# Kernel tuning notes

Hardware: AMD Instinct MI355X
Metric: run time of the kernel (lower is better)

## Reference

```python
import jax, jax.numpy as jnp
import numpy as np

L, B = 1024, 64
VALID_FRAC = 0.9  # fraction of residues with nonzero (observed) coordinates in y


def setup_inputs() -> dict:
    key = jax.random.key(0)
    kx, ky = jax.random.split(key)
    x = jax.random.normal(kx, (L, B, 3), dtype=jnp.float32)
    y = jax.random.normal(ky, (L, B, 3), dtype=jnp.float32)
    # zero out trailing residues in y so the dynamic mask (co.sum() != 0) is exercised
    valid = (jnp.arange(L) < int(VALID_FRAC * L))[:, None, None]
    y = y * valid.astype(jnp.float32)
    return {"x": x, "y": y}


def _masked_pair_dist(pts, pair_mask):
    # pts: [B, L, 3]; pair_mask: [B, L, L] (False on diagonal and on padded rows/cols)
    sq = jnp.sum(pts * pts, axis=-1)                                   # [B, L]
    d2 = sq[:, :, None] + sq[:, None, :] - 2.0 * jnp.einsum('bld,bmd->blm', pts, pts)
    d2 = jnp.maximum(d2, 0.0)                                          # relu, matches F.relu
    safe = jnp.where(pair_mask, d2, 1.0)                               # keep sqrt grad finite
    return jnp.where(pair_mask, jnp.sqrt(safe), 0.0)


def reference(x, y):
    # x, y: [L, B, 3] -> permute to [B, L, 3] as in the torch module
    xb = jnp.transpose(x, (1, 0, 2))
    yb = jnp.transpose(y, (1, 0, 2))
    Bn, Ln = xb.shape[0], xb.shape[1]
    # mask: residues of y whose coordinate sum is nonzero (index_select in original)
    mask = (jnp.sum(yb, axis=-1) != 0)                                 # [B, L]
    off_diag = ~jnp.eye(Ln, dtype=bool)
    pair_mask = mask[:, :, None] & mask[:, None, :] & off_diag         # [B, L, L]
    xd = _masked_pair_dist(xb, pair_mask)
    yd = _masked_pair_dist(yb, pair_mask)
    D = yd - xd                                                        # [B, L, L]
    per_batch = jnp.sqrt(jnp.sum(D * D, axis=(1, 2)))                  # Frobenius norm per batch
    denom = (Ln ** 2 / 2 - Ln) ** 0.5                                  # x.size(1)**2/2 - x.size(1)
    out = jnp.sum(per_batch) / denom / Bn
    return out.reshape(1)
```

## Files before the change

kernel.cpp:

```cpp
#include <hip/hip_runtime.h>
#include <math.h>

#define Lp 1024
#define Bp 64
#define Tt 128
#define NTILE 8
#define NPAIR 36

typedef float v2 __attribute__((ext_vector_type(2)));
static __device__ __forceinline__ v2 splat2(float s) { v2 r; r.x = s; r.y = s; return r; }
static __device__ __forceinline__ v2 lo2(float4 v)   { v2 r; r.x = v.x; r.y = v.y; return r; }
static __device__ __forceinline__ v2 hi2(float4 v)   { v2 r; r.x = v.z; r.y = v.w; return r; }

__global__ __launch_bounds__(256) void drmsd_main(
    const float* __restrict__ x, const float* __restrict__ y,
    float* __restrict__ partials, float* __restrict__ moments)
{
    __shared__ __align__(16) float xsx[2][Tt], xsy[2][Tt], xsz[2][Tt];
    __shared__ __align__(16) float ysx[2][Tt], ysy[2][Tt], ysz[2][Tt];
    __shared__ __align__(16) float nhx[2][Tt], nhy[2][Tt];
    __shared__ __align__(16) float ms[2][Tt];
    __shared__ float red[4];
    __shared__ float mred[4][9];

    const int b = blockIdx.x;
    const int p = blockIdx.y;
    const int t = threadIdx.x;

    if (p == NPAIR) {
        float v[9];
#pragma unroll
        for (int k = 0; k < 9; ++k) v[k] = 0.0f;
#pragma unroll
        for (int k = 0; k < 4; ++k) {
            const int row = t + k * 256;
            const float* px = x + (size_t)row * (Bp * 3) + (size_t)b * 3;
            const float* py = y + (size_t)row * (Bp * 3) + (size_t)b * 3;
            const float x0 = px[0], x1 = px[1], x2 = px[2];
            const float y0 = py[0], y1 = py[1], y2 = py[2];
            const float m = ((y0 + y1 + y2) != 0.0f) ? 1.0f : 0.0f;
            v[0] += m * x0; v[1] += m * x1; v[2] += m * x2;
            v[3] = fmaf(m, fmaf(x0, x0, fmaf(x1, x1, x2 * x2)), v[3]);
            v[4] += m * y0; v[5] += m * y1; v[6] += m * y2;
            v[7] = fmaf(m, fmaf(y0, y0, fmaf(y1, y1, y2 * y2)), v[7]);
            v[8] += m;
        }
#pragma unroll
        for (int k = 0; k < 9; ++k) {
#pragma unroll
            for (int off = 32; off > 0; off >>= 1)
                v[k] += __shfl_down(v[k], off, 64);
        }
        const int wave = t >> 6;
        if ((t & 63) == 0) {
#pragma unroll
            for (int k = 0; k < 9; ++k) mred[wave][k] = v[k];
        }
        __syncthreads();
        if (t < 9)
            moments[(size_t)b * 9 + t] =
                mred[0][t] + mred[1][t] + mred[2][t] + mred[3][t];
        return;
    }

    int ti = 0, base = 0;
    while (p >= base + (NTILE - ti)) { base += (NTILE - ti); ++ti; }
    const int tj = ti + (p - base);

    {
        const int r     = t & (Tt - 1);
        const int which = t >> 7;
        const int tile  = which ? tj : ti;
        const int row   = tile * Tt + r;
        const float* px = x + (size_t)row * (Bp * 3) + (size_t)b * 3;
        const float* py = y + (size_t)row * (Bp * 3) + (size_t)b * 3;
        const float x0 = px[0], x1 = px[1], x2 = px[2];
        const float y0 = py[0], y1 = py[1], y2 = py[2];
        xsx[which][r] = x0; xsy[which][r] = x1; xsz[which][r] = x2;
        ysx[which][r] = y0; ysy[which][r] = y1; ysz[which][r] = y2;
        nhx[which][r] = -0.5f * fmaf(x0, x0, fmaf(x1, x1, x2 * x2));
        nhy[which][r] = -0.5f * fmaf(y0, y0, fmaf(y1, y1, y2 * y2));
        ms[which][r]  = ((y0 + y1 + y2) != 0.0f) ? 1.0f : 0.0f;
    }
    __syncthreads();

    const int jc = (t & 15) << 2;
    const int rg = t >> 4;

    float total = 0.0f;

#pragma unroll
    for (int half = 0; half < 2; ++half) {
        const int i0 = half * 64 + rg * 4;
        const float4 v_xx = *(const float4*)&xsx[0][i0];
        const float4 v_xy = *(const float4*)&xsy[0][i0];
        const float4 v_xz = *(const float4*)&xsz[0][i0];
        const float4 v_yx = *(const float4*)&ysx[0][i0];
        const float4 v_yy = *(const float4*)&ysy[0][i0];
        const float4 v_yz = *(const float4*)&ysz[0][i0];
        const float4 v_hx = *(const float4*)&nhx[0][i0];
        const float4 v_hy = *(const float4*)&nhy[0][i0];
        const float4 v_mi = *(const float4*)&ms[0][i0];
        const float xix[4] = { v_xx.x, v_xx.y, v_xx.z, v_xx.w };
        const float xiy[4] = { v_xy.x, v_xy.y, v_xy.z, v_xy.w };
        const float xiz[4] = { v_xz.x, v_xz.y, v_xz.z, v_xz.w };
        const float yix[4] = { v_yx.x, v_yx.y, v_yx.z, v_yx.w };
        const float yiy[4] = { v_yy.x, v_yy.y, v_yy.z, v_yy.w };
        const float yiz[4] = { v_yz.x, v_yz.y, v_yz.z, v_yz.w };
        const float hxi[4] = { v_hx.x, v_hx.y, v_hx.z, v_hx.w };
        const float hyi[4] = { v_hy.x, v_hy.y, v_hy.z, v_hy.w };
        const float mir[4] = { v_mi.x, v_mi.y, v_mi.z, v_mi.w };

        v2 acc[4];
#pragma unroll
        for (int r = 0; r < 4; ++r) acc[r] = splat2(0.0f);

#pragma unroll
        for (int jj = 0; jj < 2; ++jj) {
            const int j0 = jj * 64 + jc;
            const float4 xjx4 = *(const float4*)&xsx[1][j0];
            const float4 xjy4 = *(const float4*)&xsy[1][j0];
            const float4 xjz4 = *(const float4*)&xsz[1][j0];
            const float4 yjx4 = *(const float4*)&ysx[1][j0];
            const float4 yjy4 = *(const float4*)&ysy[1][j0];
            const float4 yjz4 = *(const float4*)&ysz[1][j0];
            const float4 hxj4 = *(const float4*)&nhx[1][j0];
            const float4 hyj4 = *(const float4*)&nhy[1][j0];
            const float4 mj4  = *(const float4*)&ms[1][j0];
#pragma unroll
            for (int s = 0; s < 2; ++s) {
                const v2 xjx = s ? hi2(xjx4) : lo2(xjx4);
                const v2 xjy = s ? hi2(xjy4) : lo2(xjy4);
                const v2 xjz = s ? hi2(xjz4) : lo2(xjz4);
                const v2 yjx = s ? hi2(yjx4) : lo2(yjx4);
                const v2 yjy = s ? hi2(yjy4) : lo2(yjy4);
                const v2 yjz = s ? hi2(yjz4) : lo2(yjz4);
                const v2 hxj = s ? hi2(hxj4) : lo2(hxj4);
                const v2 hyj = s ? hi2(hyj4) : lo2(hyj4);
                const v2 mj  = s ? hi2(mj4)  : lo2(mj4);
#pragma unroll
                for (int r = 0; r < 4; ++r) {
                    v2 ux = splat2(hxi[r]) + hxj;
                    ux = splat2(xix[r]) * xjx + ux;
                    ux = splat2(xiy[r]) * xjy + ux;
                    ux = splat2(xiz[r]) * xjz + ux;
                    v2 uy = splat2(hyi[r]) + hyj;
                    uy = splat2(yix[r]) * yjx + uy;
                    uy = splat2(yiy[r]) * yjy + uy;
                    uy = splat2(yiz[r]) * yjz + uy;
                    const v2 pr = ux * uy;
                    v2 sq;
                    sq.x = __builtin_amdgcn_sqrtf(__builtin_fabsf(pr.x));
                    sq.y = __builtin_amdgcn_sqrtf(__builtin_fabsf(pr.y));
                    acc[r] = mj * sq + acc[r];
                }
            }
        }
#pragma unroll
        for (int r = 0; r < 4; ++r)
            total = fmaf(acc[r].x + acc[r].y, mir[r], total);
    }

#pragma unroll
    for (int off = 32; off > 0; off >>= 1)
        total += __shfl_down(total, off, 64);
    const int wave = t >> 6;
    if ((t & 63) == 0) red[wave] = total;
    __syncthreads();
    if (t == 0) {
        float s = red[0] + red[1] + red[2] + red[3];
        s *= (ti != tj) ? 4.0f : 2.0f;
        partials[(size_t)p * Bp + b] = s;
    }
}

__global__ __launch_bounds__(64) void drmsd_final(
    const float* __restrict__ partials, const float* __restrict__ moments,
    float* __restrict__ out)
{
    const int b = threadIdx.x;
    double cross = 0.0;
#pragma unroll
    for (int pp = 0; pp < NPAIR; ++pp)
        cross += (double)partials[(size_t)pp * Bp + b];

    const float* mo = moments + (size_t)b * 9;
    const double sx0 = mo[0], sx1 = mo[1], sx2 = mo[2], qx = mo[3];
    const double sy0 = mo[4], sy1 = mo[5], sy2 = mo[6], qy = mo[7];
    const double M   = mo[8];
    const double term1 = 2.0 * M * (qx + qy)
        - 2.0 * (sx0*sx0 + sx1*sx1 + sx2*sx2 + sy0*sy0 + sy1*sy1 + sy2*sy2);

    double su = term1 - 2.0 * cross;
    su = su > 0.0 ? su : 0.0;
    double pb = sqrt(su);
#pragma unroll
    for (int off = 32; off > 0; off >>= 1)
        pb += __shfl_down(pb, off, 64);
    if (b == 0) {
        const double denom = sqrt((double)Lp * (double)Lp / 2.0 - (double)Lp);
        out[0] = (float)(pb / denom / (double)Bp);
    }
}

extern "C" void kernel_launch(void* const* d_in, const int* in_sizes, int n_in,
                              void* d_out, int out_size, void* d_ws, size_t ws_size,
                              hipStream_t stream) {
    const float* x = (const float*)d_in[0];
    const float* y = (const float*)d_in[1];
    float* out      = (float*)d_out;
    float* partials = (float*)d_ws;
    float* moments  = partials + NPAIR * Bp;

    dim3 grid(Bp, NPAIR + 1);
    drmsd_main<<<grid, 256, 0, stream>>>(x, y, partials, moments);
    drmsd_final<<<1, 64, 0, stream>>>(partials, moments, out);
}
```

Baseline: 69.17 us.

## Add prep kernel for packed coordinates and fold final reduction into main via atomic ticket

A new prep kernel turns the strided [L,B,3] inputs into per-batch float4 arrays that carry the coordinates plus the negated half squared norm, along with a mask array and per-tile partial moments. The main kernel then loads these packed arrays instead of doing strided 3-float gathers and recomputing norms. The separate final kernel is removed: the last block to finish, found through an atomic counter, does the cross-batch reduction. This removes the moments block row and one launch, but adds a prep launch, an extra workspace write and read pass, and threadfence and atomic overhead in every block.

```diff
diff --git a/kernel.cpp b/kernel.cpp
--- a/kernel.cpp
+++ b/kernel.cpp
@@ -6,62 +6,77 @@
 #define Tt 128
 #define NTILE 8
 #define NPAIR 36
+#define NBLK (Bp * NPAIR)
 
 typedef float v2 __attribute__((ext_vector_type(2)));
 static __device__ __forceinline__ v2 splat2(float s) { v2 r; r.x = s; r.y = s; return r; }
 static __device__ __forceinline__ v2 lo2(float4 v)   { v2 r; r.x = v.x; r.y = v.y; return r; }
 static __device__ __forceinline__ v2 hi2(float4 v)   { v2 r; r.x = v.z; r.y = v.w; return r; }
 
+__global__ __launch_bounds__(128) void drmsd_prep(
+    const float* __restrict__ x, const float* __restrict__ y,
+    float4* __restrict__ xt, float4* __restrict__ yt,
+    float* __restrict__ msb, float* __restrict__ moments,
+    int* __restrict__ counter)
+{
+    __shared__ float mred[2][9];
+    const int b = blockIdx.x;
+    const int s = blockIdx.y;
+    const int t = threadIdx.x;
+
+    if (b == 0 && s == 0 && t == 0) *counter = 0;
+
+    const int row = s * Tt + t;
+    const float* px = x + (size_t)row * (Bp * 3) + (size_t)b * 3;
+    const float* py = y + (size_t)row * (Bp * 3) + (size_t)b * 3;
+    const float x0 = px[0], x1 = px[1], x2 = px[2];
+    const float y0 = py[0], y1 = py[1], y2 = py[2];
+    const float qxr = fmaf(x0, x0, fmaf(x1, x1, x2 * x2));
+    const float qyr = fmaf(y0, y0, fmaf(y1, y1, y2 * y2));
+    const float m   = ((y0 + y1 + y2) != 0.0f) ? 1.0f : 0.0f;
+
+    float4 rx; rx.x = x0; rx.y = x1; rx.z = x2; rx.w = -0.5f * qxr;
+    float4 ry; ry.x = y0; ry.y = y1; ry.z = y2; ry.w = -0.5f * qyr;
+    xt[(size_t)b * Lp + row] = rx;
+    yt[(size_t)b * Lp + row] = ry;
+    msb[(size_t)b * Lp + row] = m;
+
+    float v[9];
+    v[0] = m * x0; v[1] = m * x1; v[2] = m * x2; v[3] = m * qxr;
+    v[4] = m * y0; v[5] = m * y1; v[6] = m * y2; v[7] = m * qyr;
+    v[8] = m;
+#pragma unroll
+    for (int k = 0; k < 9; ++k) {
+#pragma unroll
+        for (int off = 32; off > 0; off >>= 1)
+            v[k] += __shfl_down(v[k], off, 64);
+    }
+    const int wave = t >> 6;
+    if ((t & 63) == 0) {
+#pragma unroll
+        for (int k = 0; k < 9; ++k) mred[wave][k] = v[k];
+    }
+    __syncthreads();
+    if (t < 9)
+        moments[(size_t)(s * 9 + t) * Bp + b] = mred[0][t] + mred[1][t];
+}
+
 __global__ __launch_bounds__(256) void drmsd_main(
-    const float* __restrict__ x, const float* __restrict__ y,
-    float* __restrict__ partials, float* __restrict__ moments)
+    const float4* __restrict__ xt, const float4* __restrict__ yt,
+    const float* __restrict__ msb,
+    float* __restrict__ partials, const float* __restrict__ moments,
+    int* __restrict__ counter, float* __restrict__ out)
 {
     __shared__ __align__(16) float xsx[2][Tt], xsy[2][Tt], xsz[2][Tt];
     __shared__ __align__(16) float ysx[2][Tt], ysy[2][Tt], ysz[2][Tt];
     __shared__ __align__(16) float nhx[2][Tt], nhy[2][Tt];
     __shared__ __align__(16) float ms[2][Tt];
     __shared__ float red[4];
-    __shared__ float mred[4][9];
+    __shared__ int islast;
 
     const int b = blockIdx.x;
     const int p = blockIdx.y;
     const int t = threadIdx.x;
-
-    if (p == NPAIR) {
-        float v[9];
-#pragma unroll
-        for (int k = 0; k < 9; ++k) v[k] = 0.0f;
-#pragma unroll
-        for (int k = 0; k < 4; ++k) {
-            const int row = t + k * 256;
-            const float* px = x + (size_t)row * (Bp * 3) + (size_t)b * 3;
-            const float* py = y + (size_t)row * (Bp * 3) + (size_t)b * 3;
-            const float x0 = px[0], x1 = px[1], x2 = px[2];
-            const float y0 = py[0], y1 = py[1], y2 = py[2];
-            const float m = ((y0 + y1 + y2) != 0.0f) ? 1.0f : 0.0f;
-            v[0] += m * x0; v[1] += m * x1; v[2] += m * x2;
-            v[3] = fmaf(m, fmaf(x0, x0, fmaf(x1, x1, x2 * x2)), v[3]);
-            v[4] += m * y0; v[5] += m * y1; v[6] += m * y2;
-            v[7] = fmaf(m, fmaf(y0, y0, fmaf(y1, y1, y2 * y2)), v[7]);
-            v[8] += m;
-        }
-#pragma unroll
-        for (int k = 0; k < 9; ++k) {
-#pragma unroll
-            for (int off = 32; off > 0; off >>= 1)
-                v[k] += __shfl_down(v[k], off, 64);
-        }
-        const int wave = t >> 6;
-        if ((t & 63) == 0) {
-#pragma unroll
-            for (int k = 0; k < 9; ++k) mred[wave][k] = v[k];
-        }
-        __syncthreads();
-        if (t < 9)
-            moments[(size_t)b * 9 + t] =
-                mred[0][t] + mred[1][t] + mred[2][t] + mred[3][t];
-        return;
-    }
 
     int ti = 0, base = 0;
     while (p >= base + (NTILE - ti)) { base += (NTILE - ti); ++ti; }
@@ -72,15 +87,13 @@
         const int which = t >> 7;
         const int tile  = which ? tj : ti;
         const int row   = tile * Tt + r;
-        const float* px = x + (size_t)row * (Bp * 3) + (size_t)b * 3;
-        const float* py = y + (size_t)row * (Bp * 3) + (size_t)b * 3;
-        const float x0 = px[0], x1 = px[1], x2 = px[2];
-        const float y0 = py[0], y1 = py[1], y2 = py[2];
-        xsx[which][r] = x0; xsy[which][r] = x1; xsz[which][r] = x2;
-        ysx[which][r] = y0; ysy[which][r] = y1; ysz[which][r] = y2;
-        nhx[which][r] = -0.5f * fmaf(x0, x0, fmaf(x1, x1, x2 * x2));
-        nhy[which][r] = -0.5f * fmaf(y0, y0, fmaf(y1, y1, y2 * y2));
-        ms[which][r]  = ((y0 + y1 + y2) != 0.0f) ? 1.0f : 0.0f;
+        const float4 rx = xt[(size_t)b * Lp + row];
+        const float4 ry = yt[(size_t)b * Lp + row];
+        xsx[which][r] = rx.x; xsy[which][r] = rx.y; xsz[which][r] = rx.z;
+        nhx[which][r] = rx.w;
+        ysx[which][r] = ry.x; ysy[which][r] = ry.y; ysz[which][r] = ry.z;
+        nhy[which][r] = ry.w;
+        ms[which][r]  = msb[(size_t)b * Lp + row];
     }
     __syncthreads();
 
@@ -171,35 +184,45 @@
         float s = red[0] + red[1] + red[2] + red[3];
         s *= (ti != tj) ? 4.0f : 2.0f;
         partials[(size_t)p * Bp + b] = s;
-    }
-}
-
-__global__ __launch_bounds__(64) void drmsd_final(
-    const float* __restrict__ partials, const float* __restrict__ moments,
-    float* __restrict__ out)
-{
-    const int b = threadIdx.x;
-    double cross = 0.0;
-#pragma unroll
-    for (int pp = 0; pp < NPAIR; ++pp)
-        cross += (double)partials[(size_t)pp * Bp + b];
-
-    const float* mo = moments + (size_t)b * 9;
-    const double sx0 = mo[0], sx1 = mo[1], sx2 = mo[2], qx = mo[3];
-    const double sy0 = mo[4], sy1 = mo[5], sy2 = mo[6], qy = mo[7];
-    const double M   = mo[8];
-    const double term1 = 2.0 * M * (qx + qy)
-        - 2.0 * (sx0*sx0 + sx1*sx1 + sx2*sx2 + sy0*sy0 + sy1*sy1 + sy2*sy2);
-
-    double su = term1 - 2.0 * cross;
-    su = su > 0.0 ? su : 0.0;
-    double pb = sqrt(su);
-#pragma unroll
-    for (int off = 32; off > 0; off >>= 1)
-        pb += __shfl_down(pb, off, 64);
-    if (b == 0) {
-        const double denom = sqrt((double)Lp * (double)Lp / 2.0 - (double)Lp);
-        out[0] = (float)(pb / denom / (double)Bp);
+        __threadfence();
+        const int ticket = atomicAdd(counter, 1);
+        islast = (ticket == NBLK - 1) ? 1 : 0;
+    }
+    __syncthreads();
+
+    if (islast) {
+        __threadfence();
+        if (t < Bp) {
+            const int bb = t;
+            double cross = 0.0;
+#pragma unroll
+            for (int pp = 0; pp < NPAIR; ++pp)
+                cross += (double)partials[(size_t)pp * Bp + bb];
+            float mo[9];
+#pragma unroll
+            for (int k = 0; k < 9; ++k) mo[k] = 0.0f;
+#pragma unroll
+            for (int s = 0; s < NTILE; ++s) {
+#pragma unroll
+                for (int k = 0; k < 9; ++k)
+                    mo[k] += moments[(size_t)(s * 9 + k) * Bp + bb];
+            }
+            const double sx0 = mo[0], sx1 = mo[1], sx2 = mo[2], qx = mo[3];
+            const double sy0 = mo[4], sy1 = mo[5], sy2 = mo[6], qy = mo[7];
+            const double M   = mo[8];
+            const double term1 = 2.0 * M * (qx + qy)
+                - 2.0 * (sx0*sx0 + sx1*sx1 + sx2*sx2 + sy0*sy0 + sy1*sy1 + sy2*sy2);
+            double su = term1 - 2.0 * cross;
+            su = su > 0.0 ? su : 0.0;
+            double pb = sqrt(su);
+#pragma unroll
+            for (int off = 32; off > 0; off >>= 1)
+                pb += __shfl_down(pb, off, 64);
+            if (t == 0) {
+                const double denom = sqrt((double)Lp * (double)Lp / 2.0 - (double)Lp);
+                out[0] = (float)(pb / denom / (double)Bp);
+            }
+        }
     }
 }
 
@@ -208,11 +231,18 @@
                               hipStream_t stream) {
     const float* x = (const float*)d_in[0];
     const float* y = (const float*)d_in[1];
-    float* out      = (float*)d_out;
-    float* partials = (float*)d_ws;
-    float* moments  = partials + NPAIR * Bp;
-
-    dim3 grid(Bp, NPAIR + 1);
-    drmsd_main<<<grid, 256, 0, stream>>>(x, y, partials, moments);
-    drmsd_final<<<1, 64, 0, stream>>>(partials, moments, out);
+    float* out = (float*)d_out;
+
+    float4* xt = (float4*)d_ws;
+    float4* yt = xt + (size_t)Bp * Lp;
+    float*  msb = (float*)(yt + (size_t)Bp * Lp);
+    float*  partials = msb + (size_t)Bp * Lp;
+    float*  moments  = partials + NPAIR * Bp;
+    int*    counter  = (int*)(moments + NTILE * 9 * Bp);
+
+    dim3 gprep(Bp, NTILE);
+    drmsd_prep<<<gprep, 128, 0, stream>>>(x, y, xt, yt, msb, moments, counter);
+    dim3 gmain(Bp, NPAIR);
+    drmsd_main<<<gmain, 256, 0, stream>>>(xt, yt, msb, partials, moments,
+                                          counter, out);
 }
```

After: 104.2 us. 50.7% more time.
